# Optimization experiments

Measured on AMD Instinct MI355X. Metric: run time of the kernel, lower is better.

## Reference

```python
import jax, jax.numpy as jnp
import numpy as np

N = 50000      # nodes
E = 800000     # edges (avg degree 16)
F_IN = 64      # node_features (== GENConv out, so no input projection)
H = 64         # hidden
EXP = 2 * H    # GENConv MLP expansion dim = 128
D2 = F_IN + H  # dense-block concat dim = SAGEConv in = 128
EPS_MSG = 1e-7 # GENConv message eps
BN_EPS = 1e-5


def setup_inputs() -> dict:
    key = jax.random.key(0)
    ks = jax.random.split(key, 16)
    g = lambda k, shape, fan: jax.random.normal(k, shape, jnp.float32) / np.sqrt(fan)
    return {
        "x": jax.random.normal(ks[0], (N, F_IN), jnp.float32),
        "edge_index": jax.random.randint(ks[1], (2, E), 0, N, jnp.int32),
        # GENConv MLP: Linear(64,128) -> BatchNorm(128) -> ReLU -> Linear(128,64)
        "W1": g(ks[2], (H, EXP), H), "b1": jnp.zeros((EXP,), jnp.float32),
        "gamma": jnp.ones((EXP,), jnp.float32), "beta": jnp.zeros((EXP,), jnp.float32),
        "W2": g(ks[3], (EXP, H), EXP), "b2": jnp.zeros((H,), jnp.float32),
        # SAGEConv project Linear(128,128), lin_l Linear(128,64), lin_r Linear(128,64,bias=False)
        "Wp": g(ks[4], (D2, D2), D2), "bp": jnp.zeros((D2,), jnp.float32),
        "Wl": g(ks[5], (D2, H), D2), "bl": jnp.zeros((H,), jnp.float32),
        "Wr": g(ks[6], (D2, H), D2),
        # fc Linear(64,1)
        "Wf": g(ks[7], (H, 1), H), "bf": jnp.zeros((1,), jnp.float32),
    }


def _forward(x, W1, b1, gamma, beta, W2, b2, Wp, bp, Wl, bl, Wr, Wf, bf, src, dst):
    n = x.shape[0]
    # ---- GENConv(aggr='softmax', t=1.0): msg = relu(x_j) + eps -------------
    msg = jax.nn.relu(x[src]) + EPS_MSG                       # [E, H]
    mmax = jax.ops.segment_max(msg, dst, num_segments=n)      # per-dst, per-feature max
    mmax = jax.lax.stop_gradient(jnp.where(jnp.isfinite(mmax), mmax, 0.0))
    e = jnp.exp(msg - mmax[dst])                              # t = 1.0
    denom = jax.ops.segment_sum(e, dst, num_segments=n)
    numer = jax.ops.segment_sum(e * msg, dst, num_segments=n)
    agg = numer / jnp.where(denom > 0, denom, 1.0)            # softmax aggregation
    out = agg + x                                             # residual with x_dst
    # GENConv MLP (BatchNorm in training mode: batch stats, biased var)
    h = out @ W1 + b1
    mu = h.mean(axis=0)
    var = h.var(axis=0)
    h = (h - mu) * jax.lax.rsqrt(var + BN_EPS) * gamma + beta
    h = jax.nn.relu(h) @ W2 + b2                              # [N, H]
    # ---- DeepGCNLayer block='dense': concat input ---------------------------
    x2 = jnp.concatenate([x, h], axis=-1)                     # [N, F_IN+H]
    x2 = jax.nn.sigmoid(x2)                                   # self.relu = Sigmoid()
    # ---- SAGEConv(project=True, aggr=DeepSetsAggregation()==sum) -----------
    xp = jax.nn.relu(x2 @ Wp + bp)                            # projected source feats
    aggr = jax.ops.segment_sum(xp[src], dst, num_segments=n)  # DeepSets w/o nns = sum
    out2 = aggr @ Wl + bl + x2 @ Wr                           # root uses UNprojected x2
    out2 = jax.nn.sigmoid(out2)
    logits = out2 @ Wf + bf                                   # [N, 1]
    probs = jax.nn.sigmoid(logits)                            # training branch
    return probs, logits


def reference(x, edge_index, W1, b1, gamma, beta, W2, b2, Wp, bp, Wl, bl, Wr, Wf, bf):
    src, dst = edge_index[0], edge_index[1]
    return _forward(x, W1, b1, gamma, beta, W2, b2, Wp, bp, Wl, bl, Wr, Wf, bf, src, dst)
```

## Files before the change

kernel.cpp:

```cpp
#include <hip/hip_runtime.h>

#define F_IN 64
#define HID 64
#define EXPD 128
#define D2 128
#define MAXDEG 64
#define NBW 128
#define NB 391
#define NBINB 98
#define SUBCAP 64
#define EPT 32

typedef __attribute__((ext_vector_type(8))) short bf16x8;
typedef __attribute__((ext_vector_type(4))) float f32x4;

__device__ __forceinline__ float sigmoidf_(float x) {
    return 1.0f / (1.0f + __expf(-x));
}
__device__ __forceinline__ unsigned bf16rne_(float f) {
    unsigned u = __float_as_uint(f);
    return (u + 0x7FFFu + ((u >> 16) & 1u)) >> 16;
}
__device__ __forceinline__ float bf16tof_(unsigned u16) {
    return __uint_as_float(u16 << 16);
}

__global__ __launch_bounds__(256) void k_bin(const int* __restrict__ ei,
                                             int* __restrict__ cnt2,
                                             unsigned* __restrict__ binned2,
                                             const float* __restrict__ x,
                                             unsigned short* __restrict__ x16,
                                             const float* __restrict__ W1,
                                             const float* __restrict__ W2,
                                             const float* __restrict__ Wp,
                                             const float* __restrict__ Wl,
                                             const float* __restrict__ Wr,
                                             short* __restrict__ dst,
                                             float* __restrict__ bnsums,
                                             int nE, int n, int nbinb) {
    int b = blockIdx.x;
    int tid = threadIdx.x;
    if (b < nbinb) {
        __shared__ int hist[NB];
        if (b == 0) bnsums[tid] = 0.f;
        for (int i = tid; i < NB; i += 256) hist[i] = 0;
        __syncthreads();
        unsigned ed[EPT];
        unsigned short rk[EPT];
        int e0 = b * (256 * EPT);
#pragma unroll
        for (int j = 0; j < EPT; ++j) {
            int e = e0 + j * 256 + tid;
            if (e < nE) {
                unsigned s = (unsigned)ei[e];
                unsigned d = (unsigned)ei[nE + e];
                ed[j] = s | (d << 16);
                rk[j] = (unsigned short)atomicAdd(&hist[d >> 7], 1);
            }
        }
        __syncthreads();
        for (int i = tid; i < NB; i += 256) cnt2[b * NB + i] = hist[i];
#pragma unroll
        for (int j = 0; j < EPT; ++j) {
            int e = e0 + j * 256 + tid;
            if (e < nE) {
                int bin = (ed[j] >> 16) >> 7;
                int r = (int)rk[j];
                if (r < SUBCAP)
                    binned2[((size_t)bin * nbinb + b) * SUBCAP + r] = ed[j];
            }
        }
        return;
    }
    b -= nbinb;
    if (b < 192) {
        int e = b * 256 + tid;
        const float* src;
        int K, N, base2;
        if (e < 8192)       { src = W1; K = 64;  N = 128; base2 = 0; }
        else if (e < 16384) { src = W2; K = 128; N = 64;  base2 = 8192; }
        else if (e < 32768) { src = Wp; K = 128; N = 128; base2 = 16384; }
        else if (e < 40960) { src = Wl; K = 128; N = 64;  base2 = 32768; }
        else                { src = Wr; K = 128; N = 64;  base2 = 40960; }
        int le = e - base2;
        int j = le & 7;
        int lane = (le >> 3) & 63;
        int n16 = lane & 15, q = lane >> 4;
        int rest = le >> 9;
        int KC = K / 32;
        int kc = rest % KC, nt = rest / KC;
        int k = kc * 32 + q * 8 + j;
        int col = nt * 16 + n16;
        dst[e] = (short)bf16rne_(src[(size_t)k * N + col]);
        return;
    }
    int i0 = (b - 192) * 1024 + tid * 4;
    if (i0 < n * F_IN) {
        float4 v = *(const float4*)(x + i0);
        uint2 pk;
        pk.x = bf16rne_(v.x) | (bf16rne_(v.y) << 16);
        pk.y = bf16rne_(v.z) | (bf16rne_(v.w) << 16);
        *(uint2*)(x16 + i0) = pk;
    }
}

__global__ __launch_bounds__(256) void k_csr(const int* __restrict__ cnt2,
                                             const unsigned* __restrict__ binned2,
                                             int* __restrict__ counts,
                                             unsigned short* __restrict__ csr,
                                             int n, int nbinb) {
    __shared__ unsigned short lcsr[NBW * MAXDEG];
    __shared__ int lcnt[NBW];
    __shared__ int scnt[NBINB];
    int b = blockIdx.x;
    int tid = threadIdx.x;
    if (tid < NBW) lcnt[tid] = 0;
    for (int i = tid; i < nbinb; i += 256) {
        int c = cnt2[i * NB + b];
        scnt[i] = c < SUBCAP ? c : SUBCAP;
    }
    __syncthreads();
    const unsigned* src = binned2 + (size_t)b * nbinb * SUBCAP;
    int tot = nbinb * SUBCAP;
    for (int i = tid; i < tot; i += 256) {
        int blk = i >> 6;
        int r = i & (SUBCAP - 1);
        if (r < scnt[blk]) {
            unsigned u = src[i];
            int dl = (int)(u >> 16) - b * NBW;
            int slot = atomicAdd(&lcnt[dl], 1);
            if (slot < MAXDEG) lcsr[dl * MAXDEG + slot] = (unsigned short)(u & 0xFFFF);
        }
    }
    __syncthreads();
    int nodebase = b * NBW;
    if (tid < NBW && nodebase + tid < n) counts[nodebase + tid] = lcnt[tid];
    int nrows = n - nodebase;
    nrows = nrows < NBW ? nrows : NBW;
    int nu4 = nrows * 8;
    uint4* dstrow = (uint4*)(csr + (size_t)nodebase * MAXDEG);
    for (int idx = tid; idx < nu4; idx += 256) dstrow[idx] = ((const uint4*)lcsr)[idx];
}

__global__ __launch_bounds__(256) void k_geng(const unsigned short* __restrict__ x16,
                                              const int* __restrict__ counts,
                                              const unsigned short* __restrict__ csr,
                                              const short* __restrict__ Wf,
                                              const float* __restrict__ b1,
                                              unsigned short* __restrict__ h16,
                                              float* __restrict__ bnsums, int n) {
    __shared__ short As[64 * 64];
    __shared__ float bnred[256];
    const unsigned* x32 = (const unsigned*)x16;
    int tid = threadIdx.x;
    int w = tid >> 6;
    int lane = tid & 63;
    int H = lane >> 5, f2 = lane & 31;
    int rblk = blockIdx.x * 64;
    bnred[tid] = 0.f;
    for (int t = 0; t < 16; ++t) {
        int rr = w * 16 + t;
        int v = rblk + rr;
        int q8 = f2 >> 2;
        int slot = ((rr >> 4) * 2 + (q8 >> 2)) * 64 + (q8 & 3) * 16 + (rr & 15);
        if (v < n) {
            int deg = counts[v];
            deg = deg > MAXDEG ? MAXDEG : deg;
            int idx = 0;
            if (lane < deg) idx = (int)csr[(size_t)v * MAXDEG + lane];
            float d0 = 0.f, d1 = 0.f, n0 = 0.f, n1 = 0.f;
            int i = 0;
            for (; i + 8 <= deg; i += 8) {
                int sA = __shfl(idx, i + 0 + H, 64);
                int sB = __shfl(idx, i + 2 + H, 64);
                int sC = __shfl(idx, i + 4 + H, 64);
                int sD = __shfl(idx, i + 6 + H, 64);
                unsigned uA = x32[(size_t)sA * 32 + f2];
                unsigned uB = x32[(size_t)sB * 32 + f2];
                unsigned uC = x32[(size_t)sC * 32 + f2];
                unsigned uD = x32[(size_t)sD * 32 + f2];
#pragma unroll
                for (int tt = 0; tt < 4; ++tt) {
                    unsigned u = tt == 0 ? uA : tt == 1 ? uB : tt == 2 ? uC : uD;
                    float m0 = fmaxf(bf16tof_(u & 0xFFFF), 0.f) + 1e-7f;
                    float m1 = fmaxf(bf16tof_(u >> 16), 0.f) + 1e-7f;
                    float e0 = __expf(m0), e1 = __expf(m1);
                    d0 += e0; d1 += e1;
                    n0 = fmaf(e0, m0, n0);
                    n1 = fmaf(e1, m1, n1);
                }
            }
            for (; i + 2 <= deg; i += 2) {
                int s = __shfl(idx, i + H, 64);
                unsigned u = x32[(size_t)s * 32 + f2];
                float m0 = fmaxf(bf16tof_(u & 0xFFFF), 0.f) + 1e-7f;
                float m1 = fmaxf(bf16tof_(u >> 16), 0.f) + 1e-7f;
                float e0 = __expf(m0), e1 = __expf(m1);
                d0 += e0; d1 += e1;
                n0 = fmaf(e0, m0, n0);
                n1 = fmaf(e1, m1, n1);
            }
            if (i < deg) {
                int s = __shfl(idx, i, 64);
                if (H == 0) {
                    unsigned u = x32[(size_t)s * 32 + f2];
                    float m0 = fmaxf(bf16tof_(u & 0xFFFF), 0.f) + 1e-7f;
                    float m1 = fmaxf(bf16tof_(u >> 16), 0.f) + 1e-7f;
                    float e0 = __expf(m0), e1 = __expf(m1);
                    d0 += e0; d1 += e1;
                    n0 = fmaf(e0, m0, n0);
                    n1 = fmaf(e1, m1, n1);
                }
            }
            d0 += __shfl_xor(d0, 32, 64);
            d1 += __shfl_xor(d1, 32, 64);
            n0 += __shfl_xor(n0, 32, 64);
            n1 += __shfl_xor(n1, 32, 64);
            if (H == 0) {
                float a0 = (deg > 0) ? (n0 / d0) : 0.f;
                float a1 = (deg > 0) ? (n1 / d1) : 0.f;
                unsigned xv = x32[(size_t)v * 32 + f2];
                float r0 = a0 + bf16tof_(xv & 0xFFFF);
                float r1 = a1 + bf16tof_(xv >> 16);
                *(unsigned*)(As + slot * 8 + (f2 & 3) * 2) =
                    bf16rne_(r0) | (bf16rne_(r1) << 16);
            }
        } else {
            if (H == 0) *(unsigned*)(As + slot * 8 + (f2 & 3) * 2) = 0u;
        }
    }
    __syncthreads();
    int L = lane;
    int q = L >> 4, n16 = L & 15;
    int mt_base = (w & 1) * 2;
    int nt_base = (w >> 1) * 4;
    f32x4 acc[2][4];
#pragma unroll
    for (int mt = 0; mt < 2; ++mt)
#pragma unroll
        for (int nt = 0; nt < 4; ++nt) acc[mt][nt] = (f32x4){0.f, 0.f, 0.f, 0.f};
#pragma unroll
    for (int kc = 0; kc < 2; ++kc) {
        bf16x8 a0 = *(const bf16x8*)(As + (((mt_base + 0) * 2 + kc) * 64 + L) * 8);
        bf16x8 a1 = *(const bf16x8*)(As + (((mt_base + 1) * 2 + kc) * 64 + L) * 8);
#pragma unroll
        for (int nt = 0; nt < 4; ++nt) {
            bf16x8 b = *(const bf16x8*)(Wf + (size_t)(((nt_base + nt) * 2 + kc) * 64 + L) * 8);
            acc[0][nt] = __builtin_amdgcn_mfma_f32_16x16x32_bf16(a0, b, acc[0][nt], 0, 0, 0);
            acc[1][nt] = __builtin_amdgcn_mfma_f32_16x16x32_bf16(a1, b, acc[1][nt], 0, 0, 0);
        }
    }
#pragma unroll
    for (int nt = 0; nt < 4; ++nt) {
        int col = (nt_base + nt) * 16 + n16;
        float bv = b1[col];
        float s = 0.f, s2 = 0.f;
#pragma unroll
        for (int mt = 0; mt < 2; ++mt)
#pragma unroll
            for (int r = 0; r < 4; ++r) {
                int row = rblk + (w & 1) * 32 + mt * 16 + q * 4 + r;
                float hv = acc[mt][nt][r] + bv;
                if (row < n) {
                    h16[(size_t)row * EXPD + col] = (unsigned short)bf16rne_(hv);
                    s += hv;
                    s2 = fmaf(hv, hv, s2);
                }
            }
        s += __shfl_xor(s, 16, 64);
        s += __shfl_xor(s, 32, 64);
        s2 += __shfl_xor(s2, 16, 64);
        s2 += __shfl_xor(s2, 32, 64);
        if (q == 0) {
            atomicAdd(&bnred[col], s);
            atomicAdd(&bnred[128 + col], s2);
        }
    }
    __syncthreads();
    atomicAdd(&bnsums[tid], bnred[tid]);
}

__global__ __launch_bounds__(256) void k_mlp2ab(const unsigned short* __restrict__ h16,
                                                const float* __restrict__ bnsums,
                                                const float* __restrict__ gamma,
                                                const float* __restrict__ beta,
                                                const short* __restrict__ Wf2,
                                                const float* __restrict__ b2,
                                                const unsigned short* __restrict__ x16,
                                                const short* __restrict__ Wfp,
                                                const short* __restrict__ Wfl,
                                                const short* __restrict__ Wfr,
                                                const float* __restrict__ bp,
                                                unsigned short* __restrict__ yp16,
                                                unsigned short* __restrict__ yr16,
                                                float inv_n, int n) {
    __shared__ short Bs[64 * 128];
    __shared__ short As[64 * 128];
    __shared__ float ssl[256];
    int tid = threadIdx.x;
    int rblk = blockIdx.x * 64;
    if (tid < 128) {
        float mu = bnsums[tid] * inv_n;
        float var = fmaf(-mu, mu, bnsums[128 + tid] * inv_n);
        float rs = rsqrtf(fmaxf(var, 0.f) + 1e-5f);
        float scale = gamma[tid] * rs;
        ssl[tid] = scale;
        ssl[128 + tid] = fmaf(-mu, scale, beta[tid]);
    }
    __syncthreads();
#pragma unroll
    for (int it = 0; it < 4; ++it) {
        int c = it * 256 + tid;
        int rr = c & 63, q8 = c >> 6;
        int gr = rblk + rr;
        gr = gr < n ? gr : n - 1;
        uint4 v = *(const uint4*)(h16 + (size_t)gr * EXPD + q8 * 8);
        float4 sc1 = *(const float4*)(ssl + q8 * 8);
        float4 sc2 = *(const float4*)(ssl + q8 * 8 + 4);
        float4 sh1 = *(const float4*)(ssl + 128 + q8 * 8);
        float4 sh2 = *(const float4*)(ssl + 128 + q8 * 8 + 4);
        float o0 = fmaxf(fmaf(bf16tof_(v.x & 0xFFFF), sc1.x, sh1.x), 0.f);
        float o1 = fmaxf(fmaf(bf16tof_(v.x >> 16),    sc1.y, sh1.y), 0.f);
        float o2 = fmaxf(fmaf(bf16tof_(v.y & 0xFFFF), sc1.z, sh1.z), 0.f);
        float o3 = fmaxf(fmaf(bf16tof_(v.y >> 16),    sc1.w, sh1.w), 0.f);
        float o4 = fmaxf(fmaf(bf16tof_(v.z & 0xFFFF), sc2.x, sh2.x), 0.f);
        float o5 = fmaxf(fmaf(bf16tof_(v.z >> 16),    sc2.y, sh2.y), 0.f);
        float o6 = fmaxf(fmaf(bf16tof_(v.w & 0xFFFF), sc2.z, sh2.z), 0.f);
        float o7 = fmaxf(fmaf(bf16tof_(v.w >> 16),    sc2.w, sh2.w), 0.f);
        uint4 pk;
        pk.x = bf16rne_(o0) | (bf16rne_(o1) << 16);
        pk.y = bf16rne_(o2) | (bf16rne_(o3) << 16);
        pk.z = bf16rne_(o4) | (bf16rne_(o5) << 16);
        pk.w = bf16rne_(o6) | (bf16rne_(o7) << 16);
        int slot = ((rr >> 4) * 4 + (q8 >> 2)) * 64 + (q8 & 3) * 16 + (rr & 15);
        *(uint4*)(Bs + slot * 8) = pk;
    }
#pragma unroll
    for (int it = 0; it < 2; ++it) {
        int c = it * 256 + tid;
        int rr = c & 63, q8 = c >> 6;
        int gr = rblk + rr;
        gr = gr < n ? gr : n - 1;
        uint4 v = *(const uint4*)(x16 + (size_t)gr * F_IN + q8 * 8);
        float o0 = sigmoidf_(bf16tof_(v.x & 0xFFFF));
        float o1 = sigmoidf_(bf16tof_(v.x >> 16));
        float o2 = sigmoidf_(bf16tof_(v.y & 0xFFFF));
        float o3 = sigmoidf_(bf16tof_(v.y >> 16));
        float o4 = sigmoidf_(bf16tof_(v.z & 0xFFFF));
        float o5 = sigmoidf_(bf16tof_(v.z >> 16));
        float o6 = sigmoidf_(bf16tof_(v.w & 0xFFFF));
        float o7 = sigmoidf_(bf16tof_(v.w >> 16));
        uint4 pk;
        pk.x = bf16rne_(o0) | (bf16rne_(o1) << 16);
        pk.y = bf16rne_(o2) | (bf16rne_(o3) << 16);
        pk.z = bf16rne_(o4) | (bf16rne_(o5) << 16);
        pk.w = bf16rne_(o6) | (bf16rne_(o7) << 16);
        int slot = ((rr >> 4) * 4 + (q8 >> 2)) * 64 + (q8 & 3) * 16 + (rr & 15);
        *(uint4*)(As + slot * 8) = pk;
    }
    __syncthreads();
    int L = tid & 63, w = tid >> 6;
    int q = L >> 4, n16 = L & 15;
    {
        int mtb = (w & 1) * 2, ntb = (w >> 1) * 2;
        f32x4 acch[2][2];
#pragma unroll
        for (int mt = 0; mt < 2; ++mt)
#pragma unroll
            for (int nt = 0; nt < 2; ++nt) acch[mt][nt] = (f32x4){0.f, 0.f, 0.f, 0.f};
#pragma unroll
        for (int kc = 0; kc < 4; ++kc) {
            bf16x8 a0 = *(const bf16x8*)(Bs + (((mtb + 0) * 4 + kc) * 64 + L) * 8);
            bf16x8 a1 = *(const bf16x8*)(Bs + (((mtb + 1) * 4 + kc) * 64 + L) * 8);
#pragma unroll
            for (int nt = 0; nt < 2; ++nt) {
                bf16x8 b = *(const bf16x8*)(Wf2 + (size_t)(((ntb + nt) * 4 + kc) * 64 + L) * 8);
                acch[0][nt] = __builtin_amdgcn_mfma_f32_16x16x32_bf16(a0, b, acch[0][nt], 0, 0, 0);
                acch[1][nt] = __builtin_amdgcn_mfma_f32_16x16x32_bf16(a1, b, acch[1][nt], 0, 0, 0);
            }
        }
#pragma unroll
        for (int nt = 0; nt < 2; ++nt) {
            int col = (ntb + nt) * 16 + n16;
            float bv = b2[col];
            int q8b = 8 + (col >> 3), jb = col & 7;
#pragma unroll
            for (int mt = 0; mt < 2; ++mt)
#pragma unroll
                for (int r = 0; r < 4; ++r) {
                    int rr2 = (w & 1) * 32 + mt * 16 + q * 4 + r;
                    float hv = sigmoidf_(acch[mt][nt][r] + bv);
                    int slot = ((rr2 >> 4) * 4 + (q8b >> 2)) * 64 + (q8b & 3) * 16 + (rr2 & 15);
                    As[slot * 8 + jb] = (short)bf16rne_(hv);
                }
        }
    }
    __syncthreads();
    int mt_base = (w & 1) * 2;
    int nt_base = (w >> 1) * 4;
    f32x4 acc[2][4];
    f32x4 accr[2][2];
#pragma unroll
    for (int mt = 0; mt < 2; ++mt) {
#pragma unroll
        for (int nt = 0; nt < 4; ++nt) acc[mt][nt] = (f32x4){0.f, 0.f, 0.f, 0.f};
#pragma unroll
        for (int nt = 0; nt < 2; ++nt) accr[mt][nt] = (f32x4){0.f, 0.f, 0.f, 0.f};
    }
#pragma unroll
    for (int kc = 0; kc < 4; ++kc) {
        bf16x8 a0 = *(const bf16x8*)(As + (((mt_base + 0) * 4 + kc) * 64 + L) * 8);
        bf16x8 a1 = *(const bf16x8*)(As + (((mt_base + 1) * 4 + kc) * 64 + L) * 8);
#pragma unroll
        for (int nt = 0; nt < 4; ++nt) {
            bf16x8 b = *(const bf16x8*)(Wfp + (size_t)(((nt_base + nt) * 4 + kc) * 64 + L) * 8);
            acc[0][nt] = __builtin_amdgcn_mfma_f32_16x16x32_bf16(a0, b, acc[0][nt], 0, 0, 0);
            acc[1][nt] = __builtin_amdgcn_mfma_f32_16x16x32_bf16(a1, b, acc[1][nt], 0, 0, 0);
        }
#pragma unroll
        for (int nt = 0; nt < 2; ++nt) {
            bf16x8 b = *(const bf16x8*)(Wfr + (size_t)((((w >> 1) * 2 + nt) * 4 + kc) * 64 + L) * 8);
            accr[0][nt] = __builtin_amdgcn_mfma_f32_16x16x32_bf16(a0, b, accr[0][nt], 0, 0, 0);
            accr[1][nt] = __builtin_amdgcn_mfma_f32_16x16x32_bf16(a1, b, accr[1][nt], 0, 0, 0);
        }
    }
#pragma unroll
    for (int nt = 0; nt < 2; ++nt) {
        int col = ((w >> 1) * 2 + nt) * 16 + n16;
#pragma unroll
        for (int mt = 0; mt < 2; ++mt)
#pragma unroll
            for (int r = 0; r < 4; ++r) {
                int row = rblk + (w & 1) * 32 + mt * 16 + q * 4 + r;
                if (row < n)
                    yr16[(size_t)row * HID + col] = (unsigned short)bf16rne_(accr[mt][nt][r]);
            }
    }
#pragma unroll
    for (int nt = 0; nt < 4; ++nt) {
        int kk = (nt_base + nt) * 16 + n16;
        float bv = bp[kk];
        int q8b = kk >> 3, jb = kk & 7;
#pragma unroll
        for (int mt = 0; mt < 2; ++mt)
#pragma unroll
            for (int r = 0; r < 4; ++r) {
                int rr2 = (w & 1) * 32 + mt * 16 + q * 4 + r;
                float xv = fmaxf(acc[mt][nt][r] + bv, 0.f);
                int slot = ((rr2 >> 4) * 4 + (q8b >> 2)) * 64 + (q8b & 3) * 16 + (rr2 & 15);
                Bs[slot * 8 + jb] = (short)bf16rne_(xv);
            }
    }
    __syncthreads();
    f32x4 acc2[4];
#pragma unroll
    for (int nt = 0; nt < 4; ++nt) acc2[nt] = (f32x4){0.f, 0.f, 0.f, 0.f};
#pragma unroll
    for (int kc = 0; kc < 4; ++kc) {
        bf16x8 a = *(const bf16x8*)(Bs + ((w * 4 + kc) * 64 + L) * 8);
#pragma unroll
        for (int nt = 0; nt < 4; ++nt) {
            bf16x8 b = *(const bf16x8*)(Wfl + (size_t)((nt * 4 + kc) * 64 + L) * 8);
            acc2[nt] = __builtin_amdgcn_mfma_f32_16x16x32_bf16(a, b, acc2[nt], 0, 0, 0);
        }
    }
#pragma unroll
    for (int nt = 0; nt < 4; ++nt) {
        int col = nt * 16 + n16;
#pragma unroll
        for (int r = 0; r < 4; ++r) {
            int row = rblk + w * 16 + q * 4 + r;
            if (row < n)
                yp16[(size_t)row * HID + col] = (unsigned short)bf16rne_(acc2[nt][r]);
        }
    }
}

__global__ __launch_bounds__(256) void k_sagef(const unsigned short* __restrict__ yp16,
                                               const int* __restrict__ counts,
                                               const unsigned short* __restrict__ csr,
                                               const unsigned short* __restrict__ yr16,
                                               const float* __restrict__ bl,
                                               const float* __restrict__ Wfv,
                                               const float* __restrict__ bf,
                                               float* __restrict__ out, int n) {
    const unsigned* yp32 = (const unsigned*)yp16;
    int wid = threadIdx.x >> 6;
    int lane = threadIdx.x & 63;
    int H = lane >> 5, f2 = lane & 31;
    int v = blockIdx.x * 4 + wid;
    if (v >= n) return;
    int deg = counts[v];
    deg = deg > MAXDEG ? MAXDEG : deg;
    int idx = 0;
    if (lane < deg) idx = (int)csr[(size_t)v * MAXDEG + lane];
    float a0 = 0.f, a1 = 0.f;
    int i = 0;
    for (; i + 8 <= deg; i += 8) {
        int sA = __shfl(idx, i + 0 + H, 64);
        int sB = __shfl(idx, i + 2 + H, 64);
        int sC = __shfl(idx, i + 4 + H, 64);
        int sD = __shfl(idx, i + 6 + H, 64);
        unsigned uA = yp32[(size_t)sA * 32 + f2];
        unsigned uB = yp32[(size_t)sB * 32 + f2];
        unsigned uC = yp32[(size_t)sC * 32 + f2];
        unsigned uD = yp32[(size_t)sD * 32 + f2];
        a0 += bf16tof_(uA & 0xFFFF) + bf16tof_(uB & 0xFFFF) +
              bf16tof_(uC & 0xFFFF) + bf16tof_(uD & 0xFFFF);
        a1 += bf16tof_(uA >> 16) + bf16tof_(uB >> 16) +
              bf16tof_(uC >> 16) + bf16tof_(uD >> 16);
    }
    for (; i + 2 <= deg; i += 2) {
        int s = __shfl(idx, i + H, 64);
        unsigned u = yp32[(size_t)s * 32 + f2];
        a0 += bf16tof_(u & 0xFFFF);
        a1 += bf16tof_(u >> 16);
    }
    if (i < deg) {
        int s = __shfl(idx, i, 64);
        if (H == 0) {
            unsigned u = yp32[(size_t)s * 32 + f2];
            a0 += bf16tof_(u & 0xFFFF);
            a1 += bf16tof_(u >> 16);
        }
    }
    a0 += __shfl_xor(a0, 32, 64);
    a1 += __shfl_xor(a1, 32, 64);
    if (H == 0) {
        unsigned u = ((const unsigned*)yr16)[(size_t)v * 32 + f2];
        float2 blv = ((const float2*)bl)[f2];
        float2 wv  = ((const float2*)Wfv)[f2];
        float o0 = sigmoidf_(a0 + blv.x + bf16tof_(u & 0xFFFF));
        float o1 = sigmoidf_(a1 + blv.y + bf16tof_(u >> 16));
        float t = fmaf(o0, wv.x, o1 * wv.y);
        t += __shfl_xor(t, 1, 64);
        t += __shfl_xor(t, 2, 64);
        t += __shfl_xor(t, 4, 64);
        t += __shfl_xor(t, 8, 64);
        t += __shfl_xor(t, 16, 64);
        if (f2 == 0) {
            float lg = t + bf[0];
            out[v] = sigmoidf_(lg);
            out[n + v] = lg;
        }
    }
}

extern "C" void kernel_launch(void* const* d_in, const int* in_sizes, int n_in,
                              void* d_out, int out_size, void* d_ws, size_t ws_size,
                              hipStream_t stream) {
    const float* x     = (const float*)d_in[0];
    const int*   ei    = (const int*)d_in[1];
    const float* W1    = (const float*)d_in[2];
    const float* b1    = (const float*)d_in[3];
    const float* gamma = (const float*)d_in[4];
    const float* beta  = (const float*)d_in[5];
    const float* W2    = (const float*)d_in[6];
    const float* b2    = (const float*)d_in[7];
    const float* Wp    = (const float*)d_in[8];
    const float* bp    = (const float*)d_in[9];
    const float* Wl    = (const float*)d_in[10];
    const float* bl    = (const float*)d_in[11];
    const float* Wr    = (const float*)d_in[12];
    const float* Wfv   = (const float*)d_in[13];
    const float* bf    = (const float*)d_in[14];
    const int n = in_sizes[0] / F_IN;
    const int e = in_sizes[1] / 2;

    char* ws = (char*)d_ws;
    size_t off = 0;
    auto alloc = [&](size_t bytes) -> void* {
        void* p = (void*)(ws + off);
        off += (bytes + 255) & ~(size_t)255;
        return p;
    };
    const int nbinb = (e + 256 * EPT - 1) / (256 * EPT);
    float*          bnsums   = (float*)alloc(256 * 4);
    int*            cnt2     = (int*)alloc((size_t)nbinb * NB * 4);
    int*            counts   = (int*)alloc((size_t)n * 4);
    unsigned short* csr      = (unsigned short*)alloc((size_t)n * MAXDEG * 2);
    unsigned*       binned2  = (unsigned*)alloc((size_t)NB * nbinb * SUBCAP * 4);
    unsigned short* x16      = (unsigned short*)alloc((size_t)n * F_IN * 2);
    unsigned short* h16      = (unsigned short*)alloc((size_t)n * EXPD * 2);
    unsigned short* yp16     = (unsigned short*)alloc((size_t)n * HID * 2);
    unsigned short* yr16     = (unsigned short*)alloc((size_t)n * HID * 2);
    short*          wfrag    = (short*)alloc(49152 * 2);

    float* out = (float*)d_out;
    const int nb64  = (n + 63) / 64;
    const int nb4   = (n + 3) / 4;
    const int nfp = nbinb + 192 + ((n * F_IN + 1023) / 1024);

    k_bin<<<nfp, 256, 0, stream>>>(ei, cnt2, binned2, x, x16, W1, W2, Wp, Wl,
                                   Wr, wfrag, bnsums, e, n, nbinb);
    k_csr<<<NB, 256, 0, stream>>>(cnt2, binned2, counts, csr, n, nbinb);
    k_geng<<<nb64, 256, 0, stream>>>(x16, counts, csr, wfrag, b1, h16, bnsums, n);
    k_mlp2ab<<<nb64, 256, 0, stream>>>(h16, bnsums, gamma, beta, wfrag + 8192, b2,
                                       x16, wfrag + 16384, wfrag + 32768,
                                       wfrag + 40960, bp, yp16, yr16,
                                       1.0f / (float)n, n);
    k_sagef<<<nb4, 256, 0, stream>>>(yp16, counts, csr, yr16, bl, Wfv, bf, out, n);
}
```

Measured before the change: 229.6 us.

## Split fused GENConv aggregation and first GEMM into separate kernels

```diff
diff --git a/kernel.cpp b/kernel.cpp
--- a/kernel.cpp
+++ b/kernel.cpp
@@ -142,95 +142,101 @@
     for (int idx = tid; idx < nu4; idx += 256) dstrow[idx] = ((const uint4*)lcsr)[idx];
 }
 
-__global__ __launch_bounds__(256) void k_geng(const unsigned short* __restrict__ x16,
-                                              const int* __restrict__ counts,
-                                              const unsigned short* __restrict__ csr,
-                                              const short* __restrict__ Wf,
-                                              const float* __restrict__ b1,
-                                              unsigned short* __restrict__ h16,
-                                              float* __restrict__ bnsums, int n) {
+__global__ __launch_bounds__(256) void k_gen(const unsigned short* __restrict__ x16,
+                                             const int* __restrict__ counts,
+                                             const unsigned short* __restrict__ csr,
+                                             unsigned short* __restrict__ gen16, int n) {
+    const unsigned* x32 = (const unsigned*)x16;
+    int wid = threadIdx.x >> 6;
+    int lane = threadIdx.x & 63;
+    int H = lane >> 5, f2 = lane & 31;
+    int v = blockIdx.x * 4 + wid;
+    if (v >= n) return;
+    int deg = counts[v];
+    deg = deg > MAXDEG ? MAXDEG : deg;
+    int idx = 0;
+    if (lane < deg) idx = (int)csr[(size_t)v * MAXDEG + lane];
+    float d0 = 0.f, d1 = 0.f, n0 = 0.f, n1 = 0.f;
+    int i = 0;
+    for (; i + 8 <= deg; i += 8) {
+        int sA = __shfl(idx, i + 0 + H, 64);
+        int sB = __shfl(idx, i + 2 + H, 64);
+        int sC = __shfl(idx, i + 4 + H, 64);
+        int sD = __shfl(idx, i + 6 + H, 64);
+        unsigned uA = x32[(size_t)sA * 32 + f2];
+        unsigned uB = x32[(size_t)sB * 32 + f2];
+        unsigned uC = x32[(size_t)sC * 32 + f2];
+        unsigned uD = x32[(size_t)sD * 32 + f2];
+#pragma unroll
+        for (int t = 0; t < 4; ++t) {
+            unsigned u = t == 0 ? uA : t == 1 ? uB : t == 2 ? uC : uD;
+            float m0 = fmaxf(bf16tof_(u & 0xFFFF), 0.f) + 1e-7f;
+            float m1 = fmaxf(bf16tof_(u >> 16), 0.f) + 1e-7f;
+            float e0 = __expf(m0), e1 = __expf(m1);
+            d0 += e0; d1 += e1;
+            n0 = fmaf(e0, m0, n0);
+            n1 = fmaf(e1, m1, n1);
+        }
+    }
+    for (; i + 2 <= deg; i += 2) {
+        int s = __shfl(idx, i + H, 64);
+        unsigned u = x32[(size_t)s * 32 + f2];
+        float m0 = fmaxf(bf16tof_(u & 0xFFFF), 0.f) + 1e-7f;
+        float m1 = fmaxf(bf16tof_(u >> 16), 0.f) + 1e-7f;
+        float e0 = __expf(m0), e1 = __expf(m1);
+        d0 += e0; d1 += e1;
+        n0 = fmaf(e0, m0, n0);
+        n1 = fmaf(e1, m1, n1);
+    }
+    if (i < deg) {
+        int s = __shfl(idx, i, 64);
+        if (H == 0) {
+            unsigned u = x32[(size_t)s * 32 + f2];
+            float m0 = fmaxf(bf16tof_(u & 0xFFFF), 0.f) + 1e-7f;
+            float m1 = fmaxf(bf16tof_(u >> 16), 0.f) + 1e-7f;
+            float e0 = __expf(m0), e1 = __expf(m1);
+            d0 += e0; d1 += e1;
+            n0 = fmaf(e0, m0, n0);
+            n1 = fmaf(e1, m1, n1);
+        }
+    }
+    d0 += __shfl_xor(d0, 32, 64);
+    d1 += __shfl_xor(d1, 32, 64);
+    n0 += __shfl_xor(n0, 32, 64);
+    n1 += __shfl_xor(n1, 32, 64);
+    if (H == 0) {
+        float a0 = (deg > 0) ? (n0 / d0) : 0.f;
+        float a1 = (deg > 0) ? (n1 / d1) : 0.f;
+        unsigned xv = x32[(size_t)v * 32 + f2];
+        float r0 = a0 + bf16tof_(xv & 0xFFFF);
+        float r1 = a1 + bf16tof_(xv >> 16);
+        ((unsigned*)gen16)[(size_t)v * 32 + f2] =
+            bf16rne_(r0) | (bf16rne_(r1) << 16);
+    }
+}
+
+__global__ __launch_bounds__(256) void k_gemm1(const unsigned short* __restrict__ gen16,
+                                               const short* __restrict__ Wf,
+                                               const float* __restrict__ b1,
+                                               unsigned short* __restrict__ h16,
+                                               float* __restrict__ bnsums, int n) {
     __shared__ short As[64 * 64];
     __shared__ float bnred[256];
-    const unsigned* x32 = (const unsigned*)x16;
     int tid = threadIdx.x;
-    int w = tid >> 6;
-    int lane = tid & 63;
-    int H = lane >> 5, f2 = lane & 31;
     int rblk = blockIdx.x * 64;
-    bnred[tid] = 0.f;
-    for (int t = 0; t < 16; ++t) {
-        int rr = w * 16 + t;
-        int v = rblk + rr;
-        int q8 = f2 >> 2;
+    if (tid < 256) bnred[tid] = 0.f;
+#pragma unroll
+    for (int it = 0; it < 2; ++it) {
+        int c = it * 256 + tid;
+        int rr = c & 63, q8 = c >> 6;
+        int gr = rblk + rr;
+        gr = gr < n ? gr : n - 1;
+        uint4 v = *(const uint4*)(gen16 + (size_t)gr * F_IN + q8 * 8);
         int slot = ((rr >> 4) * 2 + (q8 >> 2)) * 64 + (q8 & 3) * 16 + (rr & 15);
-        if (v < n) {
-            int deg = counts[v];
-            deg = deg > MAXDEG ? MAXDEG : deg;
-            int idx = 0;
-            if (lane < deg) idx = (int)csr[(size_t)v * MAXDEG + lane];
-            float d0 = 0.f, d1 = 0.f, n0 = 0.f, n1 = 0.f;
-            int i = 0;
-            for (; i + 8 <= deg; i += 8) {
-                int sA = __shfl(idx, i + 0 + H, 64);
-                int sB = __shfl(idx, i + 2 + H, 64);
-                int sC = __shfl(idx, i + 4 + H, 64);
-                int sD = __shfl(idx, i + 6 + H, 64);
-                unsigned uA = x32[(size_t)sA * 32 + f2];
-                unsigned uB = x32[(size_t)sB * 32 + f2];
-                unsigned uC = x32[(size_t)sC * 32 + f2];
-                unsigned uD = x32[(size_t)sD * 32 + f2];
-#pragma unroll
-                for (int tt = 0; tt < 4; ++tt) {
-                    unsigned u = tt == 0 ? uA : tt == 1 ? uB : tt == 2 ? uC : uD;
-                    float m0 = fmaxf(bf16tof_(u & 0xFFFF), 0.f) + 1e-7f;
-                    float m1 = fmaxf(bf16tof_(u >> 16), 0.f) + 1e-7f;
-                    float e0 = __expf(m0), e1 = __expf(m1);
-                    d0 += e0; d1 += e1;
-                    n0 = fmaf(e0, m0, n0);
-                    n1 = fmaf(e1, m1, n1);
-                }
-            }
-            for (; i + 2 <= deg; i += 2) {
-                int s = __shfl(idx, i + H, 64);
-                unsigned u = x32[(size_t)s * 32 + f2];
-                float m0 = fmaxf(bf16tof_(u & 0xFFFF), 0.f) + 1e-7f;
-                float m1 = fmaxf(bf16tof_(u >> 16), 0.f) + 1e-7f;
-                float e0 = __expf(m0), e1 = __expf(m1);
-                d0 += e0; d1 += e1;
-                n0 = fmaf(e0, m0, n0);
-                n1 = fmaf(e1, m1, n1);
-            }
-            if (i < deg) {
-                int s = __shfl(idx, i, 64);
-                if (H == 0) {
-                    unsigned u = x32[(size_t)s * 32 + f2];
-                    float m0 = fmaxf(bf16tof_(u & 0xFFFF), 0.f) + 1e-7f;
-                    float m1 = fmaxf(bf16tof_(u >> 16), 0.f) + 1e-7f;
-                    float e0 = __expf(m0), e1 = __expf(m1);
-                    d0 += e0; d1 += e1;
-                    n0 = fmaf(e0, m0, n0);
-                    n1 = fmaf(e1, m1, n1);
-                }
-            }
-            d0 += __shfl_xor(d0, 32, 64);
-            d1 += __shfl_xor(d1, 32, 64);
-            n0 += __shfl_xor(n0, 32, 64);
-            n1 += __shfl_xor(n1, 32, 64);
-            if (H == 0) {
-                float a0 = (deg > 0) ? (n0 / d0) : 0.f;
-                float a1 = (deg > 0) ? (n1 / d1) : 0.f;
-                unsigned xv = x32[(size_t)v * 32 + f2];
-                float r0 = a0 + bf16tof_(xv & 0xFFFF);
-                float r1 = a1 + bf16tof_(xv >> 16);
-                *(unsigned*)(As + slot * 8 + (f2 & 3) * 2) =
-                    bf16rne_(r0) | (bf16rne_(r1) << 16);
-            }
-        } else {
-            if (H == 0) *(unsigned*)(As + slot * 8 + (f2 & 3) * 2) = 0u;
-        }
-    }
-    __syncthreads();
-    int L = lane;
+        *(uint4*)(As + slot * 8) = v;
+    }
+    __syncthreads();
+    int L = tid & 63, w = tid >> 6;
     int q = L >> 4, n16 = L & 15;
     int mt_base = (w & 1) * 2;
     int nt_base = (w >> 1) * 4;
@@ -277,7 +283,7 @@
         }
     }
     __syncthreads();
-    atomicAdd(&bnsums[tid], bnred[tid]);
+    if (tid < 256) atomicAdd(&bnsums[tid], bnred[tid]);
 }
 
 __global__ __launch_bounds__(256) void k_mlp2ab(const unsigned short* __restrict__ h16,
@@ -581,6 +587,7 @@
     unsigned short* csr      = (unsigned short*)alloc((size_t)n * MAXDEG * 2);
     unsigned*       binned2  = (unsigned*)alloc((size_t)NB * nbinb * SUBCAP * 4);
     unsigned short* x16      = (unsigned short*)alloc((size_t)n * F_IN * 2);
+    unsigned short* gen16    = (unsigned short*)alloc((size_t)n * F_IN * 2);
     unsigned short* h16      = (unsigned short*)alloc((size_t)n * EXPD * 2);
     unsigned short* yp16     = (unsigned short*)alloc((size_t)n * HID * 2);
     unsigned short* yr16     = (unsigned short*)alloc((size_t)n * HID * 2);
@@ -594,7 +601,8 @@
     k_bin<<<nfp, 256, 0, stream>>>(ei, cnt2, binned2, x, x16, W1, W2, Wp, Wl,
                                    Wr, wfrag, bnsums, e, n, nbinb);
     k_csr<<<NB, 256, 0, stream>>>(cnt2, binned2, counts, csr, n, nbinb);
-    k_geng<<<nb64, 256, 0, stream>>>(x16, counts, csr, wfrag, b1, h16, bnsums, n);
+    k_gen<<<nb4, 256, 0, stream>>>(x16, counts, csr, gen16, n);
+    k_gemm1<<<nb64, 256, 0, stream>>>(gen16, wfrag, b1, h16, bnsums, n);
     k_mlp2ab<<<nb64, 256, 0, stream>>>(h16, bnsums, gamma, beta, wfrag + 8192, b2,
                                        x16, wfrag + 16384, wfrag + 32768,
                                        wfrag + 40960, bp, yp16, yr16,
```

Measured after the change: 217.7 us. -5.2%, faster.
